# Kernel tuning notes

Measured on AMD Instinct MI355X. Metric: run time of the kernel, lower is better.

The kernel has to match this reference:

```python
import jax, jax.numpy as jnp
import numpy as np

N_NODES = 50000
N_EDGES = 800000
NODE_DIM = 10
EDGE_DIM = 5
HID = 64


def _tconv(x, src, dst, e_attr, wq, bq, wk, bk, wv, bv, we, ws, bs):
    # PyG TransformerConv, heads=1, concat=True, root_weight=True, beta=False
    n = x.shape[0]
    q = x @ wq + bq                      # [N, HID]
    k = x @ wk + bk                      # [N, HID]
    v = x @ wv + bv                      # [N, HID]
    ee = e_attr @ we                     # [E, HID] (lin_edge, no bias)
    ke = k[src] + ee                     # key per edge
    ve = v[src] + ee                     # value per edge
    logits = jnp.sum(q[dst] * ke, axis=-1) / 8.0  # sqrt(64) = 8
    m = jax.ops.segment_max(logits, dst, num_segments=n)
    p = jnp.exp(logits - m[dst])
    s = jax.ops.segment_sum(p, dst, num_segments=n)
    alpha = p / s[dst]                   # segment softmax over in-neighbors
    agg = jax.ops.segment_sum(alpha[:, None] * ve, dst, num_segments=n)
    return agg + x @ ws + bs             # + lin_skip(x_i)


def setup_inputs() -> dict:
    key = jax.random.key(0)
    ks = jax.random.split(key, 32)
    x = jax.random.uniform(ks[0], (N_NODES, NODE_DIM), dtype=jnp.float32)
    edge_index = jax.random.randint(ks[1], (2, N_EDGES), 0, N_NODES, dtype=jnp.int64)
    edge_attr = jax.random.uniform(ks[2], (N_EDGES, EDGE_DIM), dtype=jnp.float32)

    def lin(k, fan_in, fan_out):
        b = 1.0 / np.sqrt(fan_in)
        return jax.random.uniform(k, (fan_in, fan_out), jnp.float32, -b, b)

    def bias(k, fan_in, fan_out):
        b = 1.0 / np.sqrt(fan_in)
        return jax.random.uniform(k, (fan_out,), jnp.float32, -b, b)

    inp = dict(x=x, edge_index=edge_index, edge_attr=edge_attr)
    # conv1: NODE_DIM -> HID
    inp['w1q'] = lin(ks[3], NODE_DIM, HID); inp['b1q'] = bias(ks[4], NODE_DIM, HID)
    inp['w1k'] = lin(ks[5], NODE_DIM, HID); inp['b1k'] = bias(ks[6], NODE_DIM, HID)
    inp['w1v'] = lin(ks[7], NODE_DIM, HID); inp['b1v'] = bias(ks[8], NODE_DIM, HID)
    inp['w1e'] = lin(ks[9], EDGE_DIM, HID)
    inp['w1s'] = lin(ks[10], NODE_DIM, HID); inp['b1s'] = bias(ks[11], NODE_DIM, HID)
    # 5 stacked HID -> HID layers
    inp['wq'] = jnp.stack([lin(jax.random.fold_in(ks[12], i), HID, HID) for i in range(5)])
    inp['bq'] = jnp.stack([bias(jax.random.fold_in(ks[13], i), HID, HID) for i in range(5)])
    inp['wk'] = jnp.stack([lin(jax.random.fold_in(ks[14], i), HID, HID) for i in range(5)])
    inp['bk'] = jnp.stack([bias(jax.random.fold_in(ks[15], i), HID, HID) for i in range(5)])
    inp['wv'] = jnp.stack([lin(jax.random.fold_in(ks[16], i), HID, HID) for i in range(5)])
    inp['bv'] = jnp.stack([bias(jax.random.fold_in(ks[17], i), HID, HID) for i in range(5)])
    inp['we'] = jnp.stack([lin(jax.random.fold_in(ks[18], i), EDGE_DIM, HID) for i in range(5)])
    inp['ws'] = jnp.stack([lin(jax.random.fold_in(ks[19], i), HID, HID) for i in range(5)])
    inp['bs'] = jnp.stack([bias(jax.random.fold_in(ks[20], i), HID, HID) for i in range(5)])
    # final linear HID -> 1
    inp['lin_w'] = lin(ks[21], HID, 1); inp['lin_b'] = bias(ks[22], HID, 1)
    return inp


def reference(x, edge_index, edge_attr, w1q, b1q, w1k, b1k, w1v, b1v, w1e, w1s, b1s,
              wq, bq, wk, bk, wv, bv, we, ws, bs, lin_w, lin_b):
    src, dst = edge_index[0], edge_index[1]  # x_j = x[src], aggregated into dst
    h = jnp.log(x + 1.0)
    e = jnp.log(edge_attr + 1.0)
    h = _tconv(h, src, dst, e, w1q, b1q, w1k, b1k, w1v, b1v, w1e, w1s, b1s)
    for i in range(5):
        h = _tconv(h, src, dst, e, wq[i], bq[i], wk[i], bk[i], wv[i], bv[i], we[i], ws[i], bs[i])
    return h @ lin_w + lin_b  # [N, 1]
```

## Files before the change

kernel.cpp:

```cpp
#include <hip/hip_runtime.h>
#include <hip/hip_fp16.h>
#include <cstdint>
#include <cstddef>

#define NN 50000
#define NE 800000
#define HD 64
#define SB 49
#define NT64 6250

__global__ void k_hist(const int* __restrict__ ei, int* __restrict__ cnt) {
    const int e0 = (blockIdx.x * blockDim.x + threadIdx.x) * 4;
    if (e0 < NE) {
        const int4 d4 = *(const int4*)(ei + NE + e0);
        atomicAdd(&cnt[d4.x], 1);
        atomicAdd(&cnt[d4.y], 1);
        atomicAdd(&cnt[d4.z], 1);
        atomicAdd(&cnt[d4.w], 1);
    }
}

__global__ __launch_bounds__(256) void k_scan1(const int* __restrict__ cnt,
                                               int* __restrict__ row_start,
                                               int* __restrict__ bsum) {
    __shared__ int ssum[256];
    const int tid = threadIdx.x, b = blockIdx.x;
    const int i0 = b * 1024 + tid * 4;
    int c0 = 0, c1 = 0, c2 = 0, c3 = 0;
    if (i0 + 3 < NN) {
        const int4 c = *(const int4*)(cnt + i0);
        c0 = c.x; c1 = c.y; c2 = c.z; c3 = c.w;
    } else {
        if (i0 + 0 < NN) c0 = cnt[i0 + 0];
        if (i0 + 1 < NN) c1 = cnt[i0 + 1];
        if (i0 + 2 < NN) c2 = cnt[i0 + 2];
        if (i0 + 3 < NN) c3 = cnt[i0 + 3];
    }
    ssum[tid] = c0 + c1 + c2 + c3;
    __syncthreads();
    for (int off = 1; off < 256; off <<= 1) {
        int v = (tid >= off) ? ssum[tid - off] : 0;
        __syncthreads();
        ssum[tid] += v;
        __syncthreads();
    }
    int ex = (tid == 0) ? 0 : ssum[tid - 1];
    if (i0 + 0 < NN) row_start[i0 + 0] = ex;
    ex += c0;
    if (i0 + 1 < NN) row_start[i0 + 1] = ex;
    ex += c1;
    if (i0 + 2 < NN) row_start[i0 + 2] = ex;
    ex += c2;
    if (i0 + 3 < NN) row_start[i0 + 3] = ex;
    if (tid == 255) bsum[b] = ssum[255];
}

__global__ __launch_bounds__(64) void k_scan2(const int* __restrict__ bsum,
                                              int* __restrict__ boff,
                                              int* __restrict__ row_start) {
    __shared__ int s[64];
    const int t = threadIdx.x;
    s[t] = (t < SB) ? bsum[t] : 0;
    __syncthreads();
    for (int off = 1; off < 64; off <<= 1) {
        int v = (t >= off) ? s[t - off] : 0;
        __syncthreads();
        s[t] += v;
        __syncthreads();
    }
    if (t < SB) boff[t] = (t == 0) ? 0 : s[t - 1];
    if (t == 0) row_start[NN] = s[SB - 1];
}

__global__ __launch_bounds__(256) void k_scan3(int* __restrict__ row_start,
                                               const int* __restrict__ boff,
                                               int* __restrict__ cur) {
    const int b = blockIdx.x;
    const int i0 = b * 1024 + threadIdx.x * 4;
    const int o = boff[b];
#pragma unroll
    for (int k = 0; k < 4; ++k) {
        int i = i0 + k;
        if (i < NN) {
            int v = row_start[i] + o;
            row_start[i] = v;
            cur[i] = v;
        }
    }
}

__global__ void k_scatter(const int* __restrict__ ei, const float* __restrict__ ea,
                          int* __restrict__ cur, uint4* __restrict__ e5p) {
    const int e0 = (blockIdx.x * blockDim.x + threadIdx.x) * 4;
    if (e0 >= NE) return;
    const int4 s4 = *(const int4*)(ei + e0);
    const int4 d4 = *(const int4*)(ei + NE + e0);
    float f[20];
    *(float4*)&f[0] = *(const float4*)(ea + (size_t)e0 * 5 + 0);
    *(float4*)&f[4] = *(const float4*)(ea + (size_t)e0 * 5 + 4);
    *(float4*)&f[8] = *(const float4*)(ea + (size_t)e0 * 5 + 8);
    *(float4*)&f[12] = *(const float4*)(ea + (size_t)e0 * 5 + 12);
    *(float4*)&f[16] = *(const float4*)(ea + (size_t)e0 * 5 + 16);
    int pos[4];
    pos[0] = atomicAdd(&cur[d4.x], 1);
    pos[1] = atomicAdd(&cur[d4.y], 1);
    pos[2] = atomicAdd(&cur[d4.z], 1);
    pos[3] = atomicAdd(&cur[d4.w], 1);
    const int ss[4] = {s4.x, s4.y, s4.z, s4.w};
#pragma unroll
    for (int j = 0; j < 4; ++j) {
        const float g0 = __logf(f[j * 5 + 0] + 1.f);
        const float g1 = __logf(f[j * 5 + 1] + 1.f);
        const float g2 = __logf(f[j * 5 + 2] + 1.f);
        const float g3 = __logf(f[j * 5 + 3] + 1.f);
        const float g4 = __logf(f[j * 5 + 4] + 1.f);
        union { __half2 h; unsigned u; } c01, c23;
        c01.h = __floats2half2_rn(g0, g1);
        c23.h = __floats2half2_rn(g2, g3);
        uint4 rec;
        rec.x = c01.u;
        rec.y = c23.u;
        rec.z = ((unsigned)ss[j] << 16) |
                (unsigned)__half_as_ushort(__float2half_rn(g4));
        rec.w = 0u;
        e5p[pos[j]] = rec;
    }
}

__device__ __forceinline__ void cvt_kv(const uint4 u, float4& k4, float4& v4) {
    const float2 p0 = __half22float2(*(const __half2*)&u.x);
    const float2 p1 = __half22float2(*(const __half2*)&u.y);
    const float2 p2 = __half22float2(*(const __half2*)&u.z);
    const float2 p3 = __half22float2(*(const __half2*)&u.w);
    k4 = make_float4(p0.x, p1.x, p2.x, p3.x);
    v4 = make_float4(p0.y, p1.y, p2.y, p3.y);
}

__global__ __launch_bounds__(256, 4) void k_qkvs64(
    const float* __restrict__ h,
    const float* __restrict__ Wq, const float* __restrict__ Bq,
    const float* __restrict__ Wk, const float* __restrict__ Bk,
    const float* __restrict__ Wv, const float* __restrict__ Bv,
    const float* __restrict__ Ws, const float* __restrict__ Bs,
    float* __restrict__ qb, __half* __restrict__ kvh, float* __restrict__ sb) {
    __shared__ float xs[2][512];
    __shared__ float kls[512];
    const int lane = threadIdx.x & 63;
    const int w = threadIdx.x >> 6;
    const float* W = (w == 0) ? Wq : (w == 1) ? Ws : (w == 2) ? Wk : Wv;
    const float* B = (w == 0) ? Bq : (w == 1) ? Bs : (w == 2) ? Bk : Bv;
    const float scl = (w == 0) ? 0.125f : 1.f;
    float wr[64];
#pragma unroll
    for (int j = 0; j < 64; ++j) wr[j] = W[j * 64 + lane] * scl;
    const float bias = B[lane] * scl;

    int tile = blockIdx.x;
    {
        const float2 g = *(const float2*)(h + (size_t)tile * 512 + threadIdx.x * 2);
        *(float2*)&xs[0][threadIdx.x * 2] = g;
    }
    __syncthreads();
    int buf = 0;
    while (true) {
        const int nt = tile + gridDim.x;
        const bool more = nt < NT64;
        float2 gn;
        if (more) gn = *(const float2*)(h + (size_t)nt * 512 + threadIdx.x * 2);
        float acc[8] = {bias, bias, bias, bias, bias, bias, bias, bias};
#pragma unroll
        for (int jq = 0; jq < 16; ++jq) {
#pragma unroll
            for (int n = 0; n < 8; ++n) {
                const float4 xv = *(const float4*)&xs[buf][n * 64 + jq * 4];
                acc[n] = fmaf(xv.x, wr[jq * 4 + 0], acc[n]);
                acc[n] = fmaf(xv.y, wr[jq * 4 + 1], acc[n]);
                acc[n] = fmaf(xv.z, wr[jq * 4 + 2], acc[n]);
                acc[n] = fmaf(xv.w, wr[jq * 4 + 3], acc[n]);
            }
        }
        if (w == 2) {
#pragma unroll
            for (int n = 0; n < 8; ++n) kls[n * 64 + lane] = acc[n];
        }
        if (more) *(float2*)&xs[buf ^ 1][threadIdx.x * 2] = gn;
        __syncthreads();
        const int nb = tile * 8;
        if (w == 0) {
#pragma unroll
            for (int n = 0; n < 8; ++n) qb[(size_t)(nb + n) * 64 + lane] = acc[n];
        } else if (w == 1) {
#pragma unroll
            for (int n = 0; n < 8; ++n) sb[(size_t)(nb + n) * 64 + lane] = acc[n];
        } else if (w == 3) {
#pragma unroll
            for (int n = 0; n < 8; ++n) {
                const float kk = kls[n * 64 + lane];
                *(__half2*)(kvh + (size_t)(nb + n) * 128 + lane * 2) =
                    __floats2half2_rn(kk, acc[n]);
            }
        }
        if (!more) break;
        __syncthreads();
        tile = nt;
        buf ^= 1;
    }
}

__global__ __launch_bounds__(256, 4) void k_qkvs10(
    const float* __restrict__ x,
    const float* __restrict__ Wq, const float* __restrict__ Bq,
    const float* __restrict__ Wk, const float* __restrict__ Bk,
    const float* __restrict__ Wv, const float* __restrict__ Bv,
    const float* __restrict__ Ws, const float* __restrict__ Bs,
    float* __restrict__ qb, __half* __restrict__ kvh, float* __restrict__ sb) {
    __shared__ float xs[640];
    const int lane = threadIdx.x & 63;
    const int w = threadIdx.x >> 6;
    const bool iskv = (w == 1 || w == 3);
    const float* WA = (w == 0) ? Wq : iskv ? Wk : Ws;
    const float* BA = (w == 0) ? Bq : iskv ? Bk : Bs;
    const float scl = (w == 0) ? 0.125f : 1.f;
    float wrA[10], wrB[10];
#pragma unroll
    for (int j = 0; j < 10; ++j) {
        wrA[j] = WA[j * 64 + lane] * scl;
        wrB[j] = iskv ? Wv[j * 64 + lane] : 0.f;
    }
    const float bA = BA[lane] * scl;
    const float bB = iskv ? Bv[lane] : 0.f;
    const int tile = blockIdx.x;
    const int fbase = tile * 640;
    const int fcnt = min(640, NN * 10 - fbase);
    if (threadIdx.x * 4 < fcnt) {
        float4 v = *(const float4*)(x + (size_t)fbase + threadIdx.x * 4);
        v.x = __logf(v.x + 1.f);
        v.y = __logf(v.y + 1.f);
        v.z = __logf(v.z + 1.f);
        v.w = __logf(v.w + 1.f);
        *(float4*)&xs[threadIdx.x * 4] = v;
    }
    __syncthreads();
    const int nbase = tile * 64;
    const int nodes = min(64, NN - nbase);
    const int n0 = (w == 3) ? 32 : 0;
    const int n1 = iskv ? ((w == 1) ? min(nodes, 32) : nodes) : nodes;
    for (int n = n0; n < n1; ++n) {
        float accA = bA, accB = bB;
#pragma unroll
        for (int j = 0; j < 10; ++j) {
            const float xv = xs[n * 10 + j];
            accA = fmaf(xv, wrA[j], accA);
            accB = fmaf(xv, wrB[j], accB);
        }
        const size_t node = (size_t)(nbase + n);
        if (iskv) {
            const __half2 hv = __floats2half2_rn(accA, accB);
            *(__half2*)(kvh + node * 128 + lane * 2) = hv;
        } else if (w == 0) {
            qb[node * 64 + lane] = accA;
        } else {
            sb[node * 64 + lane] = accA;
        }
    }
}

template <bool FINAL>
__global__ __launch_bounds__(256) void k_agg(
    const float* __restrict__ q, const __half* __restrict__ kv,
    const float* __restrict__ sk, const uint4* __restrict__ e5p,
    const float* __restrict__ wE, const int* __restrict__ row_start,
    float* __restrict__ hout, const float* __restrict__ lw, const float* lb) {
    const int lane = threadIdx.x & 63;
    const int g = lane >> 4, t = lane & 15;
    const int node = __builtin_amdgcn_readfirstlane(blockIdx.x * 4 + (threadIdx.x >> 6));
    if (node >= NN) return;
    const int beg = row_start[node], end = row_start[node + 1];
    if (beg == end) {
        const float4 s4 = *(const float4*)(sk + (size_t)node * 64 + t * 4);
        if (FINAL) {
            const float4 lw4 = *(const float4*)(lw + t * 4);
            float r = s4.x * lw4.x;
            r = fmaf(s4.y, lw4.y, r);
            r = fmaf(s4.z, lw4.z, r);
            r = fmaf(s4.w, lw4.w, r);
            r += __shfl_xor(r, 1);
            r += __shfl_xor(r, 2);
            r += __shfl_xor(r, 4);
            r += __shfl_xor(r, 8);
            if (lane == 0) hout[node] = r + lb[0];
        } else if (g == 0) {
            *(float4*)(hout + (size_t)node * 64 + t * 4) = s4;
        }
        return;
    }
    const float4 q4 = *(const float4*)(q + (size_t)node * 64 + t * 4);
    float g5[5];
    {
        const float4 wg = *(const float4*)(wE + g * 64 + t * 4);
        float dc = q4.x * wg.x;
        dc = fmaf(q4.y, wg.y, dc);
        dc = fmaf(q4.z, wg.z, dc);
        dc = fmaf(q4.w, wg.w, dc);
        dc += __shfl_xor(dc, 1);
        dc += __shfl_xor(dc, 2);
        dc += __shfl_xor(dc, 4);
        dc += __shfl_xor(dc, 8);
        const float4 w4 = *(const float4*)(wE + 4 * 64 + t * 4);
        float d4 = q4.x * w4.x;
        d4 = fmaf(q4.y, w4.y, d4);
        d4 = fmaf(q4.z, w4.z, d4);
        d4 = fmaf(q4.w, w4.w, d4);
        d4 += __shfl_xor(d4, 1);
        d4 += __shfl_xor(d4, 2);
        d4 += __shfl_xor(d4, 4);
        d4 += __shfl_xor(d4, 8);
        g5[0] = __shfl(dc, 0);
        g5[1] = __shfl(dc, 16);
        g5[2] = __shfl(dc, 32);
        g5[3] = __shfl(dc, 48);
        g5[4] = __shfl(d4, 0);
    }
    float m = -1e30f, l = 0.f;
    float4 accv = {0.f, 0.f, 0.f, 0.f};
    float a50 = 0.f, a51 = 0.f, a52 = 0.f, a53 = 0.f, a54 = 0.f;
    const char* kvc = (const char*)kv;
    const int i0x = beg + g;
    const int i0 = (i0x < end) ? i0x : beg;
    uint4 r0 = e5p[i0];
    const int i1x = beg + 4 + g;
    const int i1 = (i1x < end) ? i1x : beg;
    uint4 r1 = e5p[i1];
    uint4 kv8 =
        *(const uint4*)(kvc + (size_t)((r0.z & 0xffff0000u) >> 8) + t * 16);
#pragma unroll 2
    for (int p = beg; p < end; p += 4) {
        const int nx = p + 8 + g;
        const int npp = (nx < end) ? nx : beg;
        const uint4 rn = e5p[npp];
        const uint4 nkv =
            *(const uint4*)(kvc + (size_t)((r1.z & 0xffff0000u) >> 8) + t * 16);
        const bool act = (p + g) < end;
        float4 k4, v4;
        cvt_kv(kv8, k4, v4);
        const float2 e01 = __half22float2(*(const __half2*)&r0.x);
        const float2 e23 = __half22float2(*(const __half2*)&r0.y);
        const float e4v =
            __half2float(__ushort_as_half((unsigned short)(r0.z & 0xffffu)));
        float d = q4.x * k4.x;
        d = fmaf(q4.y, k4.y, d);
        d = fmaf(q4.z, k4.z, d);
        d = fmaf(q4.w, k4.w, d);
        d += __shfl_xor(d, 1);
        d += __shfl_xor(d, 2);
        d += __shfl_xor(d, 4);
        d += __shfl_xor(d, 8);
        float d5 = g5[0] * e01.x;
        d5 = fmaf(g5[1], e01.y, d5);
        d5 = fmaf(g5[2], e23.x, d5);
        d5 = fmaf(g5[3], e23.y, d5);
        d5 = fmaf(g5[4], e4v, d5);
        const float la = act ? (d + d5) : -__builtin_inff();
        float pa = __expf(la - m);
        if (la > m + 8.f) {
            const float rs = __expf(m - la);
            l *= rs;
            accv.x *= rs;
            accv.y *= rs;
            accv.z *= rs;
            accv.w *= rs;
            a50 *= rs;
            a51 *= rs;
            a52 *= rs;
            a53 *= rs;
            a54 *= rs;
            m = la;
            pa = 1.f;
        }
        l += pa;
        accv.x = fmaf(pa, v4.x, accv.x);
        accv.y = fmaf(pa, v4.y, accv.y);
        accv.z = fmaf(pa, v4.z, accv.z);
        accv.w = fmaf(pa, v4.w, accv.w);
        a50 = fmaf(pa, e01.x, a50);
        a51 = fmaf(pa, e01.y, a51);
        a52 = fmaf(pa, e23.x, a52);
        a53 = fmaf(pa, e23.y, a53);
        a54 = fmaf(pa, e4v, a54);
        r0 = r1;
        r1 = rn;
        kv8 = nkv;
    }
    float M = fmaxf(m, __shfl_xor(m, 16));
    M = fmaxf(M, __shfl_xor(M, 32));
    const float f = __expf(m - M);
    float lz = l * f;
    lz += __shfl_xor(lz, 16);
    lz += __shfl_xor(lz, 32);
    accv.x *= f;
    accv.y *= f;
    accv.z *= f;
    accv.w *= f;
    a50 *= f;
    a51 *= f;
    a52 *= f;
    a53 *= f;
    a54 *= f;
#pragma unroll
    for (int s = 16; s <= 32; s <<= 1) {
        accv.x += __shfl_xor(accv.x, s);
        accv.y += __shfl_xor(accv.y, s);
        accv.z += __shfl_xor(accv.z, s);
        accv.w += __shfl_xor(accv.w, s);
        a50 += __shfl_xor(a50, s);
        a51 += __shfl_xor(a51, s);
        a52 += __shfl_xor(a52, s);
        a53 += __shfl_xor(a53, s);
        a54 += __shfl_xor(a54, s);
    }
    float4 t4 = accv;
    {
        const float4 w0 = *(const float4*)(wE + 0 * 64 + t * 4);
        const float4 w1 = *(const float4*)(wE + 1 * 64 + t * 4);
        const float4 w2 = *(const float4*)(wE + 2 * 64 + t * 4);
        const float4 w3 = *(const float4*)(wE + 3 * 64 + t * 4);
        const float4 w4r = *(const float4*)(wE + 4 * 64 + t * 4);
        t4.x = fmaf(a50, w0.x, t4.x);
        t4.y = fmaf(a50, w0.y, t4.y);
        t4.z = fmaf(a50, w0.z, t4.z);
        t4.w = fmaf(a50, w0.w, t4.w);
        t4.x = fmaf(a51, w1.x, t4.x);
        t4.y = fmaf(a51, w1.y, t4.y);
        t4.z = fmaf(a51, w1.z, t4.z);
        t4.w = fmaf(a51, w1.w, t4.w);
        t4.x = fmaf(a52, w2.x, t4.x);
        t4.y = fmaf(a52, w2.y, t4.y);
        t4.z = fmaf(a52, w2.z, t4.z);
        t4.w = fmaf(a52, w2.w, t4.w);
        t4.x = fmaf(a53, w3.x, t4.x);
        t4.y = fmaf(a53, w3.y, t4.y);
        t4.z = fmaf(a53, w3.z, t4.z);
        t4.w = fmaf(a53, w3.w, t4.w);
        t4.x = fmaf(a54, w4r.x, t4.x);
        t4.y = fmaf(a54, w4r.y, t4.y);
        t4.z = fmaf(a54, w4r.z, t4.z);
        t4.w = fmaf(a54, w4r.w, t4.w);
    }
    const float4 s4 = *(const float4*)(sk + (size_t)node * 64 + t * 4);
    const float rl = 1.f / lz;
    float4 o;
    o.x = fmaf(t4.x, rl, s4.x);
    o.y = fmaf(t4.y, rl, s4.y);
    o.z = fmaf(t4.z, rl, s4.z);
    o.w = fmaf(t4.w, rl, s4.w);
    if (FINAL) {
        const float4 lw4 = *(const float4*)(lw + t * 4);
        float r = o.x * lw4.x;
        r = fmaf(o.y, lw4.y, r);
        r = fmaf(o.z, lw4.z, r);
        r = fmaf(o.w, lw4.w, r);
        r += __shfl_xor(r, 1);
        r += __shfl_xor(r, 2);
        r += __shfl_xor(r, 4);
        r += __shfl_xor(r, 8);
        if (lane == 0) hout[node] = r + lb[0];
    } else if (g == 0) {
        *(float4*)(hout + (size_t)node * 64 + t * 4) = o;
    }
}

extern "C" void kernel_launch(void* const* d_in, const int* in_sizes, int n_in,
                              void* d_out, int out_size, void* d_ws, size_t ws_size,
                              hipStream_t stream) {
    const float* x = (const float*)d_in[0];
    const int* ei = (const int*)d_in[1];
    const float* ea = (const float*)d_in[2];
    const float* w1q = (const float*)d_in[3];
    const float* b1q = (const float*)d_in[4];
    const float* w1k = (const float*)d_in[5];
    const float* b1k = (const float*)d_in[6];
    const float* w1v = (const float*)d_in[7];
    const float* b1v = (const float*)d_in[8];
    const float* w1e = (const float*)d_in[9];
    const float* w1s = (const float*)d_in[10];
    const float* b1s = (const float*)d_in[11];
    const float* wq = (const float*)d_in[12];
    const float* bq = (const float*)d_in[13];
    const float* wk = (const float*)d_in[14];
    const float* bk = (const float*)d_in[15];
    const float* wv = (const float*)d_in[16];
    const float* bv = (const float*)d_in[17];
    const float* we = (const float*)d_in[18];
    const float* ws = (const float*)d_in[19];
    const float* bs = (const float*)d_in[20];
    const float* lw = (const float*)d_in[21];
    const float* lb = (const float*)d_in[22];

    uintptr_t p = (uintptr_t)d_ws;
    auto alloc = [&](size_t bytes) -> void* {
        void* r = (void*)p;
        p += (bytes + 255) & ~(size_t)255;
        return r;
    };
    uint4* e5p = (uint4*)alloc((size_t)NE * 16);
    float* hb = (float*)alloc((size_t)NN * HD * 4);
    __half* kvh = (__half*)alloc((size_t)NN * 128 * 2);
    float* qb = (float*)alloc((size_t)NN * HD * 4);
    float* sb = (float*)alloc((size_t)NN * HD * 4);
    int* row_start = (int*)alloc((size_t)(NN + 1) * 4);
    int* cnt = (int*)alloc((size_t)NN * 4);
    int* cur = (int*)alloc((size_t)NN * 4);
    int* bsum = (int*)alloc((size_t)SB * 4);
    int* boff = (int*)alloc((size_t)SB * 4);

    hipMemsetAsync(cnt, 0, (size_t)NN * 4, stream);
    const int gedge4 = (NE / 4 + 255) / 256;
    k_hist<<<gedge4, 256, 0, stream>>>(ei, cnt);
    k_scan1<<<SB, 256, 0, stream>>>(cnt, row_start, bsum);
    k_scan2<<<1, 64, 0, stream>>>(bsum, boff, row_start);
    k_scan3<<<SB, 256, 0, stream>>>(row_start, boff, cur);
    k_scatter<<<gedge4, 256, 0, stream>>>(ei, ea, cur, e5p);

    const int gg64 = 1024;
    const int gg10 = (NN + 63) / 64;
    const int agg_grid = (NN + 3) / 4;

    k_qkvs10<<<gg10, 256, 0, stream>>>(x, w1q, b1q, w1k, b1k, w1v, b1v, w1s, b1s,
                                       qb, kvh, sb);
    k_agg<false><<<agg_grid, 256, 0, stream>>>(qb, kvh, sb, e5p, w1e, row_start,
                                               hb, lw, lb);

    for (int i = 0; i < 5; ++i) {
        k_qkvs64<<<gg64, 256, 0, stream>>>(hb, wq + i * 4096, bq + i * 64,
                                           wk + i * 4096, bk + i * 64,
                                           wv + i * 4096, bv + i * 64,
                                           ws + i * 4096, bs + i * 64,
                                           qb, kvh, sb);
        if (i < 4) {
            k_agg<false><<<agg_grid, 256, 0, stream>>>(qb, kvh, sb, e5p,
                                                       we + i * 320, row_start, hb,
                                                       lw, lb);
        } else {
            k_agg<true><<<agg_grid, 256, 0, stream>>>(qb, kvh, sb, e5p,
                                                      we + i * 320, row_start,
                                                      (float*)d_out, lw, lb);
        }
    }
}
```

Before: 627.8 us.

## Replace direct CSR scatter with two-pass bucketed scatter for locality

The single random scatter of edge records into CSR order becomes a multi-pass sort. A prep kernel packs records with the destination and builds a coarse 128-node bucket histogram. A bucket pass groups records by coarse bucket, then a fine pass scatters them to their final CSR slots, so writes and atomics land in a narrow address range. This aims to improve write locality and reduce scattered atomic traffic, but adds two extra 12.8 MB buffers and extra kernel launches and passes.

```diff
diff --git a/kernel.cpp b/kernel.cpp
--- a/kernel.cpp
+++ b/kernel.cpp
@@ -8,16 +8,39 @@
 #define HD 64
 #define SB 49
 #define NT64 6250
-
-__global__ void k_hist(const int* __restrict__ ei, int* __restrict__ cnt) {
-    const int e0 = (blockIdx.x * blockDim.x + threadIdx.x) * 4;
-    if (e0 < NE) {
-        const int4 d4 = *(const int4*)(ei + NE + e0);
-        atomicAdd(&cnt[d4.x], 1);
-        atomicAdd(&cnt[d4.y], 1);
-        atomicAdd(&cnt[d4.z], 1);
-        atomicAdd(&cnt[d4.w], 1);
-    }
+#define NB 391
+#define NBP 392
+
+__global__ __launch_bounds__(256) void k_prep(const int* __restrict__ ei,
+                                              const float* __restrict__ ea,
+                                              int* __restrict__ cnt,
+                                              int* __restrict__ bcnt,
+                                              uint4* __restrict__ tmp) {
+    __shared__ int bh[NBP];
+    for (int b = threadIdx.x; b < NBP; b += 256) bh[b] = 0;
+    __syncthreads();
+    const int e = blockIdx.x * blockDim.x + threadIdx.x;
+    const int src = ei[e];
+    const int dst = ei[NE + e];
+    atomicAdd(&cnt[dst], 1);
+    atomicAdd(&bh[dst >> 7], 1);
+    const float e0 = __logf(ea[(size_t)e * 5 + 0] + 1.f);
+    const float e1 = __logf(ea[(size_t)e * 5 + 1] + 1.f);
+    const float e2 = __logf(ea[(size_t)e * 5 + 2] + 1.f);
+    const float e3 = __logf(ea[(size_t)e * 5 + 3] + 1.f);
+    const float e4 = __logf(ea[(size_t)e * 5 + 4] + 1.f);
+    union { __half2 h; unsigned u; } c01, c23;
+    c01.h = __floats2half2_rn(e0, e1);
+    c23.h = __floats2half2_rn(e2, e3);
+    uint4 rec;
+    rec.x = c01.u;
+    rec.y = c23.u;
+    rec.z = ((unsigned)src << 16) | (unsigned)__half_as_ushort(__float2half_rn(e4));
+    rec.w = (unsigned)dst;
+    tmp[e] = rec;
+    __syncthreads();
+    for (int b = threadIdx.x; b < NBP; b += 256)
+        if (bh[b]) atomicAdd(&bcnt[b], bh[b]);
 }
 
 __global__ __launch_bounds__(256) void k_scan1(const int* __restrict__ cnt,
@@ -89,42 +112,46 @@
     }
 }
 
-__global__ void k_scatter(const int* __restrict__ ei, const float* __restrict__ ea,
-                          int* __restrict__ cur, uint4* __restrict__ e5p) {
-    const int e0 = (blockIdx.x * blockDim.x + threadIdx.x) * 4;
-    if (e0 >= NE) return;
-    const int4 s4 = *(const int4*)(ei + e0);
-    const int4 d4 = *(const int4*)(ei + NE + e0);
-    float f[20];
-    *(float4*)&f[0] = *(const float4*)(ea + (size_t)e0 * 5 + 0);
-    *(float4*)&f[4] = *(const float4*)(ea + (size_t)e0 * 5 + 4);
-    *(float4*)&f[8] = *(const float4*)(ea + (size_t)e0 * 5 + 8);
-    *(float4*)&f[12] = *(const float4*)(ea + (size_t)e0 * 5 + 12);
-    *(float4*)&f[16] = *(const float4*)(ea + (size_t)e0 * 5 + 16);
-    int pos[4];
-    pos[0] = atomicAdd(&cur[d4.x], 1);
-    pos[1] = atomicAdd(&cur[d4.y], 1);
-    pos[2] = atomicAdd(&cur[d4.z], 1);
-    pos[3] = atomicAdd(&cur[d4.w], 1);
-    const int ss[4] = {s4.x, s4.y, s4.z, s4.w};
-#pragma unroll
-    for (int j = 0; j < 4; ++j) {
-        const float g0 = __logf(f[j * 5 + 0] + 1.f);
-        const float g1 = __logf(f[j * 5 + 1] + 1.f);
-        const float g2 = __logf(f[j * 5 + 2] + 1.f);
-        const float g3 = __logf(f[j * 5 + 3] + 1.f);
-        const float g4 = __logf(f[j * 5 + 4] + 1.f);
-        union { __half2 h; unsigned u; } c01, c23;
-        c01.h = __floats2half2_rn(g0, g1);
-        c23.h = __floats2half2_rn(g2, g3);
-        uint4 rec;
-        rec.x = c01.u;
-        rec.y = c23.u;
-        rec.z = ((unsigned)ss[j] << 16) |
-                (unsigned)__half_as_ushort(__float2half_rn(g4));
-        rec.w = 0u;
-        e5p[pos[j]] = rec;
-    }
+__global__ __launch_bounds__(512) void k_bscan(const int* __restrict__ bcnt,
+                                               int* __restrict__ bcur) {
+    __shared__ int s[512];
+    const int t = threadIdx.x;
+    s[t] = (t < NBP) ? bcnt[t] : 0;
+    __syncthreads();
+    for (int off = 1; off < 512; off <<= 1) {
+        int v = (t >= off) ? s[t - off] : 0;
+        __syncthreads();
+        s[t] += v;
+        __syncthreads();
+    }
+    if (t < NBP) bcur[t] = (t == 0) ? 0 : s[t - 1];
+}
+
+__global__ __launch_bounds__(256) void k_bucket(const uint4* __restrict__ tmp,
+                                                int* __restrict__ bcur,
+                                                uint4* __restrict__ tmp2) {
+    __shared__ int bh[NBP];
+    __shared__ int bbase[NBP];
+    for (int b = threadIdx.x; b < NBP; b += 256) bh[b] = 0;
+    __syncthreads();
+    const int e = blockIdx.x * blockDim.x + threadIdx.x;
+    const uint4 rec = tmp[e];
+    const int bk = (int)(rec.w >> 7);
+    const int rank = atomicAdd(&bh[bk], 1);
+    __syncthreads();
+    for (int b = threadIdx.x; b < NBP; b += 256)
+        bbase[b] = bh[b] ? atomicAdd(&bcur[b], bh[b]) : 0;
+    __syncthreads();
+    tmp2[bbase[bk] + rank] = rec;
+}
+
+__global__ __launch_bounds__(256) void k_fine(const uint4* __restrict__ tmp2,
+                                              int* __restrict__ cur,
+                                              uint4* __restrict__ e5p) {
+    const int p = blockIdx.x * blockDim.x + threadIdx.x;
+    const uint4 rec = tmp2[p];
+    const int pos = atomicAdd(&cur[(int)rec.w], 1);
+    e5p[pos] = rec;
 }
 
 __device__ __forceinline__ void cvt_kv(const uint4 u, float4& k4, float4& v4) {
@@ -503,6 +530,8 @@
         return r;
     };
     uint4* e5p = (uint4*)alloc((size_t)NE * 16);
+    uint4* tmp = (uint4*)alloc((size_t)NE * 16);
+    uint4* tmp2 = (uint4*)alloc((size_t)NE * 16);
     float* hb = (float*)alloc((size_t)NN * HD * 4);
     __half* kvh = (__half*)alloc((size_t)NN * 128 * 2);
     float* qb = (float*)alloc((size_t)NN * HD * 4);
@@ -512,14 +541,19 @@
     int* cur = (int*)alloc((size_t)NN * 4);
     int* bsum = (int*)alloc((size_t)SB * 4);
     int* boff = (int*)alloc((size_t)SB * 4);
+    int* bcnt = (int*)alloc((size_t)NBP * 4);
+    int* bcur = (int*)alloc((size_t)NBP * 4);
 
     hipMemsetAsync(cnt, 0, (size_t)NN * 4, stream);
-    const int gedge4 = (NE / 4 + 255) / 256;
-    k_hist<<<gedge4, 256, 0, stream>>>(ei, cnt);
+    hipMemsetAsync(bcnt, 0, (size_t)NBP * 4, stream);
+    const int gedge = NE / 256;
+    k_prep<<<gedge, 256, 0, stream>>>(ei, ea, cnt, bcnt, tmp);
     k_scan1<<<SB, 256, 0, stream>>>(cnt, row_start, bsum);
     k_scan2<<<1, 64, 0, stream>>>(bsum, boff, row_start);
     k_scan3<<<SB, 256, 0, stream>>>(row_start, boff, cur);
-    k_scatter<<<gedge4, 256, 0, stream>>>(ei, ea, cur, e5p);
+    k_bscan<<<1, 512, 0, stream>>>(bcnt, bcur);
+    k_bucket<<<gedge, 256, 0, stream>>>(tmp, bcur, tmp2);
+    k_fine<<<gedge, 256, 0, stream>>>(tmp2, cur, e5p);
 
     const int gg64 = 1024;
     const int gg10 = (NN + 63) / 64;
```

Result: slower. 726.5 us (+15.7%).
